# Performance work log

Hardware: AMD Instinct MI355X
Metric: run time of the kernel (lower is better)

## Reference

```python
import jax, jax.numpy as jnp
import numpy as np

D_MODEL = 1024
NUM_HEADS = 16
DEPTH = D_MODEL // NUM_HEADS
B, S = 2, 2048


def setup_inputs() -> dict:
    key = jax.random.key(0)
    ks = jax.random.split(key, 12)
    scale = 1.0 / np.sqrt(D_MODEL)
    inp = {
        "q": jax.random.normal(ks[0], (B, S, D_MODEL), dtype=jnp.float32),
        "k": jax.random.normal(ks[1], (B, S, D_MODEL), dtype=jnp.float32),
        "v": jax.random.normal(ks[2], (B, S, D_MODEL), dtype=jnp.float32),
        "mask": jax.random.uniform(ks[3], (B, 1, S, S), dtype=jnp.float32),
        # Linear params, torch convention: y = x @ W.T + b
        "Wq": jax.random.normal(ks[4], (D_MODEL, D_MODEL), dtype=jnp.float32) * scale,
        "bq": jnp.zeros((D_MODEL,), dtype=jnp.float32),
        "Wk": jax.random.normal(ks[5], (D_MODEL, D_MODEL), dtype=jnp.float32) * scale,
        "bk": jnp.zeros((D_MODEL,), dtype=jnp.float32),
        "Wv": jax.random.normal(ks[6], (D_MODEL, D_MODEL), dtype=jnp.float32) * scale,
        "bv": jnp.zeros((D_MODEL,), dtype=jnp.float32),
        "Wo": jax.random.normal(ks[7], (D_MODEL, D_MODEL), dtype=jnp.float32) * scale,
        "bo": jnp.zeros((D_MODEL,), dtype=jnp.float32),
    }
    return inp


def _split_heads(x):
    # [B, S, D] -> [B, H, S, depth]
    b, s, _ = x.shape
    return x.reshape(b, s, NUM_HEADS, DEPTH).transpose(0, 2, 1, 3)


def reference(q, k, v, mask, Wq, bq, Wk, bk, Wv, bv, Wo, bo):
    qh = _split_heads(q @ Wq.T + bq)
    kh = _split_heads(k @ Wk.T + bk)
    vh = _split_heads(v @ Wv.T + bv)
    # scaled dot-product attention, full [B,H,S,S] scores (as in source)
    logits = jnp.einsum("bhqd,bhkd->bhqk", qh, kh) / jnp.sqrt(
        jnp.asarray(DEPTH, dtype=jnp.float32)
    )
    logits = logits + mask * 1e-09  # faithful to source (mask * 1e-9)
    weights = jax.nn.softmax(logits, axis=-1)
    attn = jnp.einsum("bhqk,bhkd->bhqd", weights, vh)
    attn = attn.transpose(0, 2, 1, 3).reshape(q.shape[0], -1, D_MODEL)
    out = attn @ Wo.T + bo
    return (out, weights)
```

## Files before the change

### kernel.cpp

```cpp
#include <hip/hip_runtime.h>
#include <type_traits>


typedef _Float16 half8 __attribute__((ext_vector_type(8)));
typedef float    floatx4 __attribute__((ext_vector_type(4)));

#define MFMA16(a, b, c) __builtin_amdgcn_mfma_f32_16x16x32_f16((a), (b), (c), 0, 0, 0)

#define D_MODEL 1024
#define S_LEN   2048
#define NHEAD   16
#define DEPTH   64
#define BATCH   2

template <int MODE, typename TIN>
__global__ __launch_bounds__(256, 2) void lin_kernel(
    const TIN* __restrict__ X, const float* __restrict__ W,
    const float* __restrict__ bias, void* __restrict__ outp)
{
    __shared__ _Float16 A_lds[64 * 40];
    __shared__ _Float16 B_lds[64 * 40];

    const int tid  = threadIdx.x;
    const int lane = tid & 63;
    const int wv   = tid >> 6;
    const int r15  = lane & 15;
    const int quad = lane >> 4;
    const int bn   = blockIdx.x;
    const int bm   = blockIdx.y;
    const int srow = tid >> 2;
    const int sseg = tid & 3;

    const TIN*   ax = X + (size_t)(bm * 64 + srow) * 1024 + sseg * 8;
    const float* bx = W + (size_t)(bn * 64 + srow) * 1024 + sseg * 8;
    _Float16* asl = &A_lds[srow * 40 + sseg * 8];
    _Float16* bsl = &B_lds[srow * 40 + sseg * 8];

    floatx4 acc[4];
#pragma unroll
    for (int t = 0; t < 4; ++t) acc[t] = floatx4{0.f, 0.f, 0.f, 0.f};

    for (int k0 = 0; k0 < 1024; k0 += 32) {
        half8 av, bv8;
        if constexpr (std::is_same<TIN, _Float16>::value) {
            av = *(const half8*)(ax + k0);
        } else {
            floatx4 f0 = *(const floatx4*)(ax + k0);
            floatx4 f1 = *(const floatx4*)(ax + k0 + 4);
#pragma unroll
            for (int i = 0; i < 4; ++i) { av[i] = (_Float16)f0[i]; av[i + 4] = (_Float16)f1[i]; }
        }
        {
            floatx4 f0 = *(const floatx4*)(bx + k0);
            floatx4 f1 = *(const floatx4*)(bx + k0 + 4);
#pragma unroll
            for (int i = 0; i < 4; ++i) { bv8[i] = (_Float16)f0[i]; bv8[i + 4] = (_Float16)f1[i]; }
        }
        __syncthreads();
        *(half8*)asl = av;
        *(half8*)bsl = bv8;
        __syncthreads();
        half8 bf = *(const half8*)&B_lds[(wv * 16 + r15) * 40 + quad * 8];
#pragma unroll
        for (int t = 0; t < 4; ++t) {
            half8 af = *(const half8*)&A_lds[(t * 16 + r15) * 40 + quad * 8];
            acc[t] = MFMA16(af, bf, acc[t]);
        }
    }

    const int gcol = bn * 64 + wv * 16 + r15;
    const float bb = bias[gcol];
    if constexpr (MODE == 0) {
        _Float16* o = (_Float16*)outp;
        const int hh = gcol >> 6, dd = gcol & 63;
#pragma unroll
        for (int t = 0; t < 4; ++t) {
#pragma unroll
            for (int r = 0; r < 4; ++r) {
                int grow = bm * 64 + t * 16 + quad * 4 + r;
                int b_ = grow >> 11, s = grow & 2047;
                o[((size_t)((b_ * 16 + hh) * 2048 + s)) * 64 + dd] =
                    (_Float16)(acc[t][r] + bb);
            }
        }
    } else {
        float* o = (float*)outp;
#pragma unroll
        for (int t = 0; t < 4; ++t) {
#pragma unroll
            for (int r = 0; r < 4; ++r) {
                int grow = bm * 64 + t * 16 + quad * 4 + r;
                o[(size_t)grow * 1024 + gcol] = acc[t][r] + bb;
            }
        }
    }
}

__global__ __launch_bounds__(256, 2) void attn_kernel(
    const _Float16* __restrict__ Q, const _Float16* __restrict__ K,
    const _Float16* __restrict__ V, float* __restrict__ wout,
    _Float16* __restrict__ attn_out)
{
    __shared__ _Float16 stage[64 * 72];
    __shared__ _Float16 w_lds[16 * 2056];
    __shared__ float red[2][4][16];

    const int tid  = threadIdx.x;
    const int lane = tid & 63;
    const int wv   = tid >> 6;
    const int r15  = lane & 15;
    const int quad = lane >> 4;
    const int qb   = blockIdx.x;
    const int h    = blockIdx.y;
    const int b    = blockIdx.z;

    const size_t hoff = ((size_t)(b * 16 + h)) * S_LEN * DEPTH;
    const _Float16* Qh = Q + hoff + (size_t)qb * 16 * DEPTH;
    const _Float16* Kh = K + hoff;
    const _Float16* Vh = V + hoff;

    half8 q0 = *(const half8*)(Qh + r15 * 64 + quad * 8);
    half8 q1 = *(const half8*)(Qh + r15 * 64 + 32 + quad * 8);

    const int srow = tid >> 2;
    const int sseg = tid & 3;

    floatx4 S[32];

#pragma unroll
    for (int kt = 0; kt < 32; ++kt) {
        const _Float16* src = Kh + (size_t)(kt * 64 + srow) * 64 + sseg * 16;
        half8 v0 = *(const half8*)src;
        half8 v1 = *(const half8*)(src + 8);
        __syncthreads();
        *(half8*)&stage[srow * 72 + sseg * 16] = v0;
        *(half8*)&stage[srow * 72 + sseg * 16 + 8] = v1;
        __syncthreads();
        half8 b0 = *(const half8*)&stage[(wv * 16 + r15) * 72 + quad * 8];
        half8 b1 = *(const half8*)&stage[(wv * 16 + r15) * 72 + 32 + quad * 8];
        floatx4 z = floatx4{0.f, 0.f, 0.f, 0.f};
        z = MFMA16(q0, b0, z);
        z = MFMA16(q1, b1, z);
        S[kt] = z;
    }

    float pm[4] = {-1e30f, -1e30f, -1e30f, -1e30f};
#pragma unroll
    for (int kt = 0; kt < 32; ++kt) {
#pragma unroll
        for (int j = 0; j < 4; ++j) {
            S[kt][j] *= 0.125f;
            pm[j] = fmaxf(pm[j], S[kt][j]);
        }
    }
#pragma unroll
    for (int m = 1; m <= 8; m <<= 1) {
#pragma unroll
        for (int j = 0; j < 4; ++j) pm[j] = fmaxf(pm[j], __shfl_xor(pm[j], m, 64));
    }
#pragma unroll
    for (int j = 0; j < 4; ++j)
        if (r15 == j) red[0][wv][quad * 4 + j] = pm[j];
    __syncthreads();
    float gm[4];
#pragma unroll
    for (int j = 0; j < 4; ++j) {
        int row = quad * 4 + j;
        gm[j] = fmaxf(fmaxf(red[0][0][row], red[0][1][row]),
                      fmaxf(red[0][2][row], red[0][3][row]));
    }
    float ps[4] = {0.f, 0.f, 0.f, 0.f};
#pragma unroll
    for (int kt = 0; kt < 32; ++kt) {
#pragma unroll
        for (int j = 0; j < 4; ++j) {
            float e = __expf(S[kt][j] - gm[j]);
            S[kt][j] = e;
            ps[j] += e;
        }
    }
#pragma unroll
    for (int m = 1; m <= 8; m <<= 1) {
#pragma unroll
        for (int j = 0; j < 4; ++j) ps[j] += __shfl_xor(ps[j], m, 64);
    }
#pragma unroll
    for (int j = 0; j < 4; ++j)
        if (r15 == j) red[1][wv][quad * 4 + j] = ps[j];
    __syncthreads();
    float gl[4];
#pragma unroll
    for (int j = 0; j < 4; ++j) {
        int row = quad * 4 + j;
        gl[j] = 1.0f / (red[1][0][row] + red[1][1][row] + red[1][2][row] + red[1][3][row]);
    }

    float* wrow = wout + (((size_t)(b * 16 + h)) * S_LEN + (size_t)qb * 16) * S_LEN;
#pragma unroll
    for (int kt = 0; kt < 32; ++kt) {
#pragma unroll
        for (int j = 0; j < 4; ++j) {
            float val = S[kt][j] * gl[j];
            int row = quad * 4 + j;
            int key = kt * 64 + wv * 16 + r15;
            wrow[(size_t)row * S_LEN + key] = val;
            w_lds[row * 2056 + key] = (_Float16)val;
        }
    }
    __syncthreads();

    const int vkey  = tid & 63;
    const int vdseg = tid >> 6;
    floatx4 oacc = floatx4{0.f, 0.f, 0.f, 0.f};
    for (int vt = 0; vt < 32; ++vt) {
        const _Float16* vsrc = Vh + (size_t)(vt * 64 + vkey) * 64 + vdseg * 16;
        half8 v0 = *(const half8*)vsrc;
        half8 v1 = *(const half8*)(vsrc + 8);
        __syncthreads();
#pragma unroll
        for (int jj = 0; jj < 8; ++jj) {
            stage[(vdseg * 16 + jj) * 72 + vkey]     = v0[jj];
            stage[(vdseg * 16 + 8 + jj) * 72 + vkey] = v1[jj];
        }
        __syncthreads();
#pragma unroll
        for (int ks = 0; ks < 2; ++ks) {
            half8 af = *(const half8*)&w_lds[r15 * 2056 + vt * 64 + ks * 32 + quad * 8];
            half8 bf = *(const half8*)&stage[(wv * 16 + r15) * 72 + ks * 32 + quad * 8];
            oacc = MFMA16(af, bf, oacc);
        }
    }

    _Float16* ao = attn_out + ((size_t)(b * S_LEN + qb * 16)) * D_MODEL + h * 64 + wv * 16;
#pragma unroll
    for (int r = 0; r < 4; ++r)
        ao[(size_t)(quad * 4 + r) * D_MODEL + r15] = (_Float16)oacc[r];
}

extern "C" void kernel_launch(void* const* d_in, const int* in_sizes, int n_in,
                              void* d_out, int out_size, void* d_ws, size_t ws_size,
                              hipStream_t stream)
{
    const float* q  = (const float*)d_in[0];
    const float* k  = (const float*)d_in[1];
    const float* v  = (const float*)d_in[2];
    const float* Wq = (const float*)d_in[4];
    const float* bq = (const float*)d_in[5];
    const float* Wk = (const float*)d_in[6];
    const float* bk = (const float*)d_in[7];
    const float* Wv = (const float*)d_in[8];
    const float* bv = (const float*)d_in[9];
    const float* Wo = (const float*)d_in[10];
    const float* bo = (const float*)d_in[11];

    const size_t NTOK = (size_t)BATCH * S_LEN * D_MODEL;
    _Float16* Qw = (_Float16*)d_ws;
    _Float16* Kw = Qw + NTOK;
    _Float16* Vw = Kw + NTOK;
    _Float16* Aw = Vw + NTOK;

    float* out  = (float*)d_out;
    float* wout = out + NTOK;

    dim3 blk(256);
    dim3 lin_grid(16, 64);
    lin_kernel<0, float><<<lin_grid, blk, 0, stream>>>(q, Wq, bq, (void*)Qw);
    lin_kernel<0, float><<<lin_grid, blk, 0, stream>>>(k, Wk, bk, (void*)Kw);
    lin_kernel<0, float><<<lin_grid, blk, 0, stream>>>(v, Wv, bv, (void*)Vw);
    attn_kernel<<<dim3(128, 16, 2), blk, 0, stream>>>(Qw, Kw, Vw, wout, Aw);
    lin_kernel<1, _Float16><<<lin_grid, blk, 0, stream>>>(Aw, Wo, bo, (void*)out);
}
```

Baseline: 1.120 ms.

## Pre-convert inputs to fp16, use 128x128 GEMM tiles, transpose V for attention

```diff
diff --git a/kernel.cpp b/kernel.cpp
--- a/kernel.cpp
+++ b/kernel.cpp
@@ -1,5 +1,4 @@
 #include <hip/hip_runtime.h>
-#include <type_traits>
 
 
 typedef _Float16 half8 __attribute__((ext_vector_type(8)));
@@ -13,84 +12,101 @@
 #define DEPTH   64
 #define BATCH   2
 
-template <int MODE, typename TIN>
-__global__ __launch_bounds__(256, 2) void lin_kernel(
-    const TIN* __restrict__ X, const float* __restrict__ W,
+__device__ __forceinline__ void gld_lds16(const _Float16* g, _Float16* l) {
+    __builtin_amdgcn_global_load_lds(
+        (const __attribute__((address_space(1))) unsigned int*)g,
+        (__attribute__((address_space(3))) unsigned int*)l, 16, 0, 0);
+}
+
+__global__ void cvt_kernel(const float* __restrict__ src, _Float16* __restrict__ dst, int n8) {
+    int i = blockIdx.x * 256 + threadIdx.x;
+    if (i < n8) {
+        const floatx4* s = (const floatx4*)src + (size_t)i * 2;
+        floatx4 f0 = s[0], f1 = s[1];
+        half8 h;
+#pragma unroll
+        for (int j = 0; j < 4; ++j) { h[j] = (_Float16)f0[j]; h[4 + j] = (_Float16)f1[j]; }
+        *((half8*)dst + i) = h;
+    }
+}
+
+template <int MODE>
+__global__ __launch_bounds__(256) void gemm_kernel(
+    const _Float16* __restrict__ X, const _Float16* __restrict__ W,
     const float* __restrict__ bias, void* __restrict__ outp)
 {
-    __shared__ _Float16 A_lds[64 * 40];
-    __shared__ _Float16 B_lds[64 * 40];
+    __shared__ _Float16 A_lds[128 * 32];
+    __shared__ _Float16 B_lds[128 * 32];
 
     const int tid  = threadIdx.x;
     const int lane = tid & 63;
-    const int wv   = tid >> 6;
+    const int w    = tid >> 6;
     const int r15  = lane & 15;
     const int quad = lane >> 4;
+    const int wr   = w >> 1, wc = w & 1;
     const int bn   = blockIdx.x;
     const int bm   = blockIdx.y;
-    const int srow = tid >> 2;
-    const int sseg = tid & 3;
-
-    const TIN*   ax = X + (size_t)(bm * 64 + srow) * 1024 + sseg * 8;
-    const float* bx = W + (size_t)(bn * 64 + srow) * 1024 + sseg * 8;
-    _Float16* asl = &A_lds[srow * 40 + sseg * 8];
-    _Float16* bsl = &B_lds[srow * 40 + sseg * 8];
-
-    floatx4 acc[4];
-#pragma unroll
-    for (int t = 0; t < 4; ++t) acc[t] = floatx4{0.f, 0.f, 0.f, 0.f};
+
+    const int srow = w * 16 + (lane >> 2);
+    const int sseg = lane & 3;
+    const _Float16* ag = X + (size_t)(bm * 128 + srow) * 1024 + sseg * 8;
+    const _Float16* bg = W + (size_t)(bn * 128 + srow) * 1024 + sseg * 8;
+    _Float16* al = &A_lds[srow * 32 + sseg * 8];
+    _Float16* bl = &B_lds[srow * 32 + sseg * 8];
+
+    floatx4 acc[4][4];
+#pragma unroll
+    for (int t = 0; t < 4; ++t)
+#pragma unroll
+        for (int u = 0; u < 4; ++u) acc[t][u] = floatx4{0.f, 0.f, 0.f, 0.f};
 
     for (int k0 = 0; k0 < 1024; k0 += 32) {
-        half8 av, bv8;
-        if constexpr (std::is_same<TIN, _Float16>::value) {
-            av = *(const half8*)(ax + k0);
-        } else {
-            floatx4 f0 = *(const floatx4*)(ax + k0);
-            floatx4 f1 = *(const floatx4*)(ax + k0 + 4);
-#pragma unroll
-            for (int i = 0; i < 4; ++i) { av[i] = (_Float16)f0[i]; av[i + 4] = (_Float16)f1[i]; }
-        }
-        {
-            floatx4 f0 = *(const floatx4*)(bx + k0);
-            floatx4 f1 = *(const floatx4*)(bx + k0 + 4);
-#pragma unroll
-            for (int i = 0; i < 4; ++i) { bv8[i] = (_Float16)f0[i]; bv8[i + 4] = (_Float16)f1[i]; }
-        }
-        __syncthreads();
-        *(half8*)asl = av;
-        *(half8*)bsl = bv8;
-        __syncthreads();
-        half8 bf = *(const half8*)&B_lds[(wv * 16 + r15) * 40 + quad * 8];
-#pragma unroll
-        for (int t = 0; t < 4; ++t) {
-            half8 af = *(const half8*)&A_lds[(t * 16 + r15) * 40 + quad * 8];
-            acc[t] = MFMA16(af, bf, acc[t]);
-        }
-    }
-
-    const int gcol = bn * 64 + wv * 16 + r15;
-    const float bb = bias[gcol];
-    if constexpr (MODE == 0) {
-        _Float16* o = (_Float16*)outp;
-        const int hh = gcol >> 6, dd = gcol & 63;
-#pragma unroll
-        for (int t = 0; t < 4; ++t) {
+        __syncthreads();
+        gld_lds16(ag + k0, al);
+        gld_lds16(ag + k0 + (size_t)64 * 1024, al + 64 * 32);
+        gld_lds16(bg + k0, bl);
+        gld_lds16(bg + k0 + (size_t)64 * 1024, bl + 64 * 32);
+        __syncthreads();
+        half8 a[4], bf[4];
+#pragma unroll
+        for (int t = 0; t < 4; ++t)
+            a[t] = *(const half8*)&A_lds[(wr * 64 + t * 16 + r15) * 32 + quad * 8];
+#pragma unroll
+        for (int u = 0; u < 4; ++u)
+            bf[u] = *(const half8*)&B_lds[(wc * 64 + u * 16 + r15) * 32 + quad * 8];
+#pragma unroll
+        for (int t = 0; t < 4; ++t)
+#pragma unroll
+            for (int u = 0; u < 4; ++u) acc[t][u] = MFMA16(a[t], bf[u], acc[t][u]);
+    }
+
+    const int gc0 = bn * 128 + wc * 64;
+    float bb[4];
+#pragma unroll
+    for (int u = 0; u < 4; ++u) bb[u] = bias[gc0 + u * 16 + r15];
+
+#pragma unroll
+    for (int t = 0; t < 4; ++t) {
+#pragma unroll
+        for (int u = 0; u < 4; ++u) {
+            const int gc = gc0 + u * 16 + r15;
 #pragma unroll
             for (int r = 0; r < 4; ++r) {
-                int grow = bm * 64 + t * 16 + quad * 4 + r;
-                int b_ = grow >> 11, s = grow & 2047;
-                o[((size_t)((b_ * 16 + hh) * 2048 + s)) * 64 + dd] =
-                    (_Float16)(acc[t][r] + bb);
-            }
-        }
-    } else {
-        float* o = (float*)outp;
-#pragma unroll
-        for (int t = 0; t < 4; ++t) {
-#pragma unroll
-            for (int r = 0; r < 4; ++r) {
-                int grow = bm * 64 + t * 16 + quad * 4 + r;
-                o[(size_t)grow * 1024 + gcol] = acc[t][r] + bb;
+                const int grow = bm * 128 + wr * 64 + t * 16 + quad * 4 + r;
+                const float val = acc[t][u][r] + bb[u];
+                if constexpr (MODE == 0) {
+                    const int hh = gc >> 6, dd = gc & 63;
+                    const int b_ = grow >> 11, s = grow & 2047;
+                    ((_Float16*)outp)[((size_t)((b_ * 16 + hh) * 2048 + s)) * 64 + dd] =
+                        (_Float16)val;
+                } else if constexpr (MODE == 2) {
+                    const int hh = gc >> 6, dd = gc & 63;
+                    const int b_ = grow >> 11, s = grow & 2047;
+                    ((_Float16*)outp)[((size_t)((b_ * 16 + hh) * 64 + dd)) * 2048 + s] =
+                        (_Float16)val;
+                } else {
+                    ((float*)outp)[(size_t)grow * 1024 + gc] = val;
+                }
             }
         }
     }
@@ -98,11 +114,10 @@
 
 __global__ __launch_bounds__(256, 2) void attn_kernel(
     const _Float16* __restrict__ Q, const _Float16* __restrict__ K,
-    const _Float16* __restrict__ V, float* __restrict__ wout,
+    const _Float16* __restrict__ Vt, float* __restrict__ wout,
     _Float16* __restrict__ attn_out)
 {
-    __shared__ _Float16 stage[64 * 72];
-    __shared__ _Float16 w_lds[16 * 2056];
+    __shared__ _Float16 w_lds[16 * 1032];
     __shared__ float red[2][4][16];
 
     const int tid  = threadIdx.x;
@@ -115,29 +130,19 @@
     const int b    = blockIdx.z;
 
     const size_t hoff = ((size_t)(b * 16 + h)) * S_LEN * DEPTH;
-    const _Float16* Qh = Q + hoff + (size_t)qb * 16 * DEPTH;
-    const _Float16* Kh = K + hoff;
-    const _Float16* Vh = V + hoff;
+    const _Float16* Qh  = Q + hoff + (size_t)qb * 16 * DEPTH;
+    const _Float16* Kh  = K + hoff;
+    const _Float16* Vth = Vt + hoff;
 
     half8 q0 = *(const half8*)(Qh + r15 * 64 + quad * 8);
     half8 q1 = *(const half8*)(Qh + r15 * 64 + 32 + quad * 8);
 
-    const int srow = tid >> 2;
-    const int sseg = tid & 3;
-
     floatx4 S[32];
-
 #pragma unroll
     for (int kt = 0; kt < 32; ++kt) {
-        const _Float16* src = Kh + (size_t)(kt * 64 + srow) * 64 + sseg * 16;
-        half8 v0 = *(const half8*)src;
-        half8 v1 = *(const half8*)(src + 8);
-        __syncthreads();
-        *(half8*)&stage[srow * 72 + sseg * 16] = v0;
-        *(half8*)&stage[srow * 72 + sseg * 16 + 8] = v1;
-        __syncthreads();
-        half8 b0 = *(const half8*)&stage[(wv * 16 + r15) * 72 + quad * 8];
-        half8 b1 = *(const half8*)&stage[(wv * 16 + r15) * 72 + 32 + quad * 8];
+        const _Float16* kp = Kh + (size_t)(kt * 64 + wv * 16 + r15) * 64 + quad * 8;
+        half8 b0 = *(const half8*)kp;
+        half8 b1 = *(const half8*)(kp + 32);
         floatx4 z = floatx4{0.f, 0.f, 0.f, 0.f};
         z = MFMA16(q0, b0, z);
         z = MFMA16(q1, b1, z);
@@ -146,18 +151,16 @@
 
     float pm[4] = {-1e30f, -1e30f, -1e30f, -1e30f};
 #pragma unroll
-    for (int kt = 0; kt < 32; ++kt) {
+    for (int kt = 0; kt < 32; ++kt)
 #pragma unroll
         for (int j = 0; j < 4; ++j) {
             S[kt][j] *= 0.125f;
             pm[j] = fmaxf(pm[j], S[kt][j]);
         }
-    }
-#pragma unroll
-    for (int m = 1; m <= 8; m <<= 1) {
+#pragma unroll
+    for (int m = 1; m <= 8; m <<= 1)
 #pragma unroll
         for (int j = 0; j < 4; ++j) pm[j] = fmaxf(pm[j], __shfl_xor(pm[j], m, 64));
-    }
 #pragma unroll
     for (int j = 0; j < 4; ++j)
         if (r15 == j) red[0][wv][quad * 4 + j] = pm[j];
@@ -171,19 +174,17 @@
     }
     float ps[4] = {0.f, 0.f, 0.f, 0.f};
 #pragma unroll
-    for (int kt = 0; kt < 32; ++kt) {
+    for (int kt = 0; kt < 32; ++kt)
 #pragma unroll
         for (int j = 0; j < 4; ++j) {
             float e = __expf(S[kt][j] - gm[j]);
             S[kt][j] = e;
             ps[j] += e;
         }
-    }
-#pragma unroll
-    for (int m = 1; m <= 8; m <<= 1) {
+#pragma unroll
+    for (int m = 1; m <= 8; m <<= 1)
 #pragma unroll
         for (int j = 0; j < 4; ++j) ps[j] += __shfl_xor(ps[j], m, 64);
-    }
 #pragma unroll
     for (int j = 0; j < 4; ++j)
         if (r15 == j) red[1][wv][quad * 4 + j] = ps[j];
@@ -196,39 +197,35 @@
     }
 
     float* wrow = wout + (((size_t)(b * 16 + h)) * S_LEN + (size_t)qb * 16) * S_LEN;
-#pragma unroll
-    for (int kt = 0; kt < 32; ++kt) {
-#pragma unroll
-        for (int j = 0; j < 4; ++j) {
-            float val = S[kt][j] * gl[j];
-            int row = quad * 4 + j;
-            int key = kt * 64 + wv * 16 + r15;
-            wrow[(size_t)row * S_LEN + key] = val;
-            w_lds[row * 2056 + key] = (_Float16)val;
-        }
-    }
-    __syncthreads();
-
-    const int vkey  = tid & 63;
-    const int vdseg = tid >> 6;
     floatx4 oacc = floatx4{0.f, 0.f, 0.f, 0.f};
-    for (int vt = 0; vt < 32; ++vt) {
-        const _Float16* vsrc = Vh + (size_t)(vt * 64 + vkey) * 64 + vdseg * 16;
-        half8 v0 = *(const half8*)vsrc;
-        half8 v1 = *(const half8*)(vsrc + 8);
-        __syncthreads();
-#pragma unroll
-        for (int jj = 0; jj < 8; ++jj) {
-            stage[(vdseg * 16 + jj) * 72 + vkey]     = v0[jj];
-            stage[(vdseg * 16 + 8 + jj) * 72 + vkey] = v1[jj];
-        }
-        __syncthreads();
-#pragma unroll
-        for (int ks = 0; ks < 2; ++ks) {
-            half8 af = *(const half8*)&w_lds[r15 * 2056 + vt * 64 + ks * 32 + quad * 8];
-            half8 bf = *(const half8*)&stage[(wv * 16 + r15) * 72 + ks * 32 + quad * 8];
-            oacc = MFMA16(af, bf, oacc);
-        }
+#pragma unroll
+    for (int hf = 0; hf < 2; ++hf) {
+#pragma unroll
+        for (int k2 = 0; k2 < 16; ++k2) {
+            const int kt = hf * 16 + k2;
+#pragma unroll
+            for (int j = 0; j < 4; ++j)
+                w_lds[(quad * 4 + j) * 1032 + k2 * 64 + wv * 16 + r15] =
+                    (_Float16)(S[kt][j] * gl[j]);
+        }
+        __syncthreads();
+#pragma unroll
+        for (int k2 = 0; k2 < 16; ++k2) {
+            const int kt = hf * 16 + k2;
+#pragma unroll
+            for (int j = 0; j < 4; ++j)
+                wrow[(size_t)(quad * 4 + j) * 2048 + kt * 64 + wv * 16 + r15] =
+                    S[kt][j] * gl[j];
+            const _Float16* vp =
+                Vth + (size_t)(wv * 16 + r15) * 2048 + (size_t)kt * 64 + quad * 8;
+            half8 a0 = *(const half8*)&w_lds[r15 * 1032 + k2 * 64 + quad * 8];
+            half8 a1 = *(const half8*)&w_lds[r15 * 1032 + k2 * 64 + 32 + quad * 8];
+            half8 b0 = *(const half8*)vp;
+            half8 b1 = *(const half8*)(vp + 32);
+            oacc = MFMA16(a0, b0, oacc);
+            oacc = MFMA16(a1, b1, oacc);
+        }
+        __syncthreads();
     }
 
     _Float16* ao = attn_out + ((size_t)(b * S_LEN + qb * 16)) * D_MODEL + h * 64 + wv * 16;
@@ -254,19 +251,38 @@
     const float* bo = (const float*)d_in[11];
 
     const size_t NTOK = (size_t)BATCH * S_LEN * D_MODEL;
-    _Float16* Qw = (_Float16*)d_ws;
-    _Float16* Kw = Qw + NTOK;
-    _Float16* Vw = Kw + NTOK;
-    _Float16* Aw = Vw + NTOK;
+    const size_t WSZ  = (size_t)D_MODEL * D_MODEL;
+    _Float16* base = (_Float16*)d_ws;
+    _Float16* qh  = base;
+    _Float16* kh  = base + NTOK;
+    _Float16* vh  = base + 2 * NTOK;
+    _Float16* Qw  = base + 3 * NTOK;
+    _Float16* Kw  = base + 4 * NTOK;
+    _Float16* Vt  = base + 5 * NTOK;
+    _Float16* Wqh = base + 6 * NTOK;
+    _Float16* Wkh = Wqh + WSZ;
+    _Float16* Wvh = Wkh + WSZ;
+    _Float16* Woh = Wvh + WSZ;
+    _Float16* Aw  = qh;
 
     float* out  = (float*)d_out;
     float* wout = out + NTOK;
 
     dim3 blk(256);
-    dim3 lin_grid(16, 64);
-    lin_kernel<0, float><<<lin_grid, blk, 0, stream>>>(q, Wq, bq, (void*)Qw);
-    lin_kernel<0, float><<<lin_grid, blk, 0, stream>>>(k, Wk, bk, (void*)Kw);
-    lin_kernel<0, float><<<lin_grid, blk, 0, stream>>>(v, Wv, bv, (void*)Vw);
-    attn_kernel<<<dim3(128, 16, 2), blk, 0, stream>>>(Qw, Kw, Vw, wout, Aw);
-    lin_kernel<1, _Float16><<<lin_grid, blk, 0, stream>>>(Aw, Wo, bo, (void*)out);
-}
+    cvt_kernel<<<dim3(2048), blk, 0, stream>>>(q, qh, (int)(NTOK / 8));
+    cvt_kernel<<<dim3(2048), blk, 0, stream>>>(k, kh, (int)(NTOK / 8));
+    cvt_kernel<<<dim3(2048), blk, 0, stream>>>(v, vh, (int)(NTOK / 8));
+    cvt_kernel<<<dim3(512),  blk, 0, stream>>>(Wq, Wqh, (int)(WSZ / 8));
+    cvt_kernel<<<dim3(512),  blk, 0, stream>>>(Wk, Wkh, (int)(WSZ / 8));
+    cvt_kernel<<<dim3(512),  blk, 0, stream>>>(Wv, Wvh, (int)(WSZ / 8));
+    cvt_kernel<<<dim3(512),  blk, 0, stream>>>(Wo, Woh, (int)(WSZ / 8));
+
+    dim3 ggrid(8, 32);
+    gemm_kernel<0><<<ggrid, blk, 0, stream>>>(qh, Wqh, bq, (void*)Qw);
+    gemm_kernel<0><<<ggrid, blk, 0, stream>>>(kh, Wkh, bk, (void*)Kw);
+    gemm_kernel<2><<<ggrid, blk, 0, stream>>>(vh, Wvh, bv, (void*)Vt);
+
+    attn_kernel<<<dim3(128, 16, 2), blk, 0, stream>>>(Qw, Kw, Vt, wout, Aw);
+
+    gemm_kernel<1><<<ggrid, blk, 0, stream>>>(Aw, Woh, bo, (void*)out);
+}
```

Measured after the change: 991.9 us. 11.5% less time.
